# Optimization experiments

Hardware: AMD Instinct MI355X
Metric: run time of the kernel (lower is better)

## Reference

```python
import jax, jax.numpy as jnp
import numpy as np

# config (mirrors init_kwargs)
P_DROP = 0.5          # patch_dropout_proba
MIN_F, MAX_F = 0.1, 0.5  # min/max fraction of patches dropped
B, C, H, W = 64, 64, 128, 128
KH, KW = 8, 8
HP, WP = H // KH, W // KW   # 16, 16 (zero leftout padding since H%KH==0)
PQ = HP * WP                # 256 patches per image


def setup_inputs() -> dict:
    key = jax.random.key(0)
    kb, ke = jax.random.split(key)
    batch = jax.random.normal(kb, (B, C, H, W), dtype=jnp.float32)
    # patch_dropout_embed: torch used 2*(rand(1,C,KH,KW)-0.5) expanded to PQ copies;
    # stored here as an independent (PQ, C, KH, KW) parameter tensor.
    embed = 2.0 * (jax.random.uniform(ke, (PQ, C, KH, KW), dtype=jnp.float32) - 0.5)
    return {"batch": batch, "embed": embed}


def _swap_mask(key):
    """Vectorized per-image patch-drop mask [B, PQ] (replaces python batch loop)."""
    k1, k2, k3 = jax.random.split(key, 3)
    apply = jax.random.uniform(k1, (B,)) < P_DROP                       # per-image coin flip
    frac = jax.random.uniform(k2, (B,)) * (MAX_F - MIN_F) + MIN_F       # dropped fraction
    dropped = jnp.floor(frac * PQ).astype(jnp.int32)                    # int(frac * patch_qty)
    r = jax.random.uniform(k3, (B, PQ))
    ranks = jnp.argsort(jnp.argsort(r, axis=-1), axis=-1)               # random permutation ranks
    return (ranks < dropped[:, None]) & apply[:, None]


def reference(batch, embed):
    mask = _swap_mask(jax.random.key(42))                               # [B, PQ]
    # tile image into patches: [B, C, HP, WP, KH, KW]
    x = batch.reshape(B, C, HP, KH, WP, KW).transpose(0, 1, 2, 4, 3, 5)
    # embed.permute(1,0,2,3).view(C, HP, WP, KH, KW) from the torch code
    e = embed.transpose(1, 0, 2, 3).reshape(C, HP, WP, KH, KW)
    m = mask.reshape(B, 1, HP, WP, 1, 1)
    out = jnp.where(m, e[None], x)
    return out.transpose(0, 1, 2, 4, 3, 5).reshape(B, C, H, W)
```

## Files before the change

### kernel.cpp

```cpp
#include <hip/hip_runtime.h>
#include <stdint.h>


#define BB 64
#define PQ 256

typedef float f32x4 __attribute__((ext_vector_type(4)));

__device__ __forceinline__ uint32_t rotl32(uint32_t v, int r) {
  return (v << r) | (v >> (32 - r));
}

__device__ __forceinline__ void tf2x32(uint32_t k0, uint32_t k1,
                                       uint32_t x0, uint32_t x1,
                                       uint32_t& o0, uint32_t& o1) {
  uint32_t ks2 = k0 ^ k1 ^ 0x1BD11BDAu;
  x0 += k0; x1 += k1;
#define TFR(r) { x0 += x1; x1 = rotl32(x1, (r)); x1 ^= x0; }
  TFR(13) TFR(15) TFR(26) TFR(6)   x0 += k1;  x1 += ks2 + 1u;
  TFR(17) TFR(29) TFR(16) TFR(24)  x0 += ks2; x1 += k0  + 2u;
  TFR(13) TFR(15) TFR(26) TFR(6)   x0 += k0;  x1 += k1  + 3u;
  TFR(17) TFR(29) TFR(16) TFR(24)  x0 += k1;  x1 += ks2 + 4u;
  TFR(13) TFR(15) TFR(26) TFR(6)   x0 += ks2; x1 += k0  + 5u;
#undef TFR
  o0 = x0; o1 = x1;
}

__device__ __forceinline__ uint32_t tf_fold(uint32_t k0, uint32_t k1,
                                            uint32_t c_hi, uint32_t c_lo) {
  uint32_t a, b;
  tf2x32(k0, k1, c_hi, c_lo, a, b);
  return a ^ b;
}

__device__ __forceinline__ float bits_to_unif(uint32_t bits) {
  return __uint_as_float((bits >> 9) | 0x3f800000u) - 1.0f;
}

__global__ __launch_bounds__(256) void mask_kernel(unsigned char* __restrict__ mask) {
  __shared__ uint32_t keybits[PQ];
  __shared__ int s_dropped;
  __shared__ int s_apply;

  const int b = blockIdx.x;
  const int p = threadIdx.x;

  uint32_t k3a, k3b; tf2x32(0u, 42u, 0u, 2u, k3a, k3b);

  const uint32_t rb = tf_fold(k3a, k3b, 0u, (uint32_t)(b * PQ + p)) >> 9;
  keybits[p] = rb;

  if (p == 0) {
    uint32_t k1a, k1b; tf2x32(0u, 42u, 0u, 0u, k1a, k1b);
    uint32_t k2a, k2b; tf2x32(0u, 42u, 0u, 1u, k2a, k2b);
    float u1 = bits_to_unif(tf_fold(k1a, k1b, 0u, (uint32_t)b));
    float u2 = bits_to_unif(tf_fold(k2a, k2b, 0u, (uint32_t)b));
    s_apply = (u1 < 0.5f) ? 1 : 0;
    float frac = u2 * 0.4f;
    frac = frac + 0.1f;
    s_dropped = (int)floorf(frac * 256.0f);
  }
  __syncthreads();

  int rank = 0;
  for (int q = 0; q < PQ; ++q) {
    uint32_t o = keybits[q];
    rank += (o < rb) || (o == rb && q < p);
  }
  mask[b * PQ + p] = (s_apply && rank < s_dropped) ? 1 : 0;
}

__global__ __launch_bounds__(256) void patch_dropout_kernel(
    const f32x4* __restrict__ batch,
    const f32x4* __restrict__ embed,
    const unsigned char* __restrict__ mask,
    f32x4* __restrict__ out, int n4) {
  int i = blockIdx.x * blockDim.x + threadIdx.x;
  if (i >= n4) return;
  const int w4 = i & 31;
  const int h  = (i >> 5) & 127;
  const int c  = (i >> 12) & 63;
  const int b  = i >> 18;
  const int pq = ((h >> 3) << 4) | (w4 >> 1);

  f32x4 v;
  if (mask[(b << 8) | pq]) {
    v = embed[(pq << 10) + (c << 4) + ((h & 7) << 1) + (w4 & 1)];
  } else {
    v = batch[i];
  }
  __builtin_nontemporal_store(v, &out[i]);
}

extern "C" void kernel_launch(void* const* d_in, const int* in_sizes, int n_in,
                              void* d_out, int out_size, void* d_ws, size_t ws_size,
                              hipStream_t stream) {
  const float* batch = (const float*)d_in[0];
  const float* embed = (const float*)d_in[1];
  float* out = (float*)d_out;
  unsigned char* mask = (unsigned char*)d_ws;

  mask_kernel<<<BB, 256, 0, stream>>>(mask);

  const int n4 = out_size / 4;
  const int blocks = (n4 + 255) / 256;
  patch_dropout_kernel<<<blocks, 256, 0, stream>>>(
      (const f32x4*)batch, (const f32x4*)embed, mask, (f32x4*)out, n4);
}
```

Before: 92.02 us.

## Fuse mask generation into patch dropout kernel with per-block partial rank compute

Drops the separate mask kernel and launch. Each block of the copy kernel computes the mask bits for its 16 patches itself, using a split rank count over shared memory with shuffle reduction, and skips the RNG and rank work when the image is not selected. This removes one kernel launch, the mask round trip through global memory and the serialization between the two kernels. In exchange, every block repeats the Threefry hashing and the partial ranking, and adds barriers to the memory-bound copy path.

Measured after the change: 94.23 us. 1.02x slower.

```diff
diff --git a/kernel.cpp b/kernel.cpp
--- a/kernel.cpp
+++ b/kernel.cpp
@@ -2,8 +2,9 @@
 #include <stdint.h>
 
 
-#define BB 64
 #define PQ 256
+#define MAIN_THREADS 256
+#define MAIN_BLOCKS 65536
 
 typedef float f32x4 __attribute__((ext_vector_type(4)));
 
@@ -37,20 +38,21 @@
   return __uint_as_float((bits >> 9) | 0x3f800000u) - 1.0f;
 }
 
-__global__ __launch_bounds__(256) void mask_kernel(unsigned char* __restrict__ mask) {
+__global__ __launch_bounds__(MAIN_THREADS) void patch_dropout_fused(
+    const f32x4* __restrict__ batch,
+    const f32x4* __restrict__ embed,
+    f32x4* __restrict__ out) {
   __shared__ uint32_t keybits[PQ];
-  __shared__ int s_dropped;
-  __shared__ int s_apply;
+  __shared__ int s_m[16];
+  __shared__ int s_apply, s_dropped;
 
-  const int b = blockIdx.x;
-  const int p = threadIdx.x;
+  const int tid  = threadIdx.x;
+  const int base = blockIdx.x * MAIN_THREADS;
+  const int i    = base + tid;
+  const int b    = i >> 18;
+  const int hp0  = ((base >> 5) & 127) >> 3;
 
-  uint32_t k3a, k3b; tf2x32(0u, 42u, 0u, 2u, k3a, k3b);
-
-  const uint32_t rb = tf_fold(k3a, k3b, 0u, (uint32_t)(b * PQ + p)) >> 9;
-  keybits[p] = rb;
-
-  if (p == 0) {
+  if (tid == 0) {
     uint32_t k1a, k1b; tf2x32(0u, 42u, 0u, 0u, k1a, k1b);
     uint32_t k2a, k2b; tf2x32(0u, 42u, 0u, 1u, k2a, k2b);
     float u1 = bits_to_unif(tf_fold(k1a, k1b, 0u, (uint32_t)b));
@@ -62,29 +64,41 @@
   }
   __syncthreads();
 
-  int rank = 0;
-  for (int q = 0; q < PQ; ++q) {
-    uint32_t o = keybits[q];
-    rank += (o < rb) || (o == rb && q < p);
+  if (s_apply) {
+    uint32_t k3a, k3b; tf2x32(0u, 42u, 0u, 2u, k3a, k3b);
+    keybits[tid] = tf_fold(k3a, k3b, 0u, (uint32_t)(b * PQ + tid)) >> 9;
+    __syncthreads();
+
+    const int j = tid >> 4;
+    const int k = tid & 15;
+    const int pqj = (hp0 << 4) | j;
+    const uint32_t rp = keybits[pqj];
+    int part = 0;
+#pragma unroll
+    for (int qq = 0; qq < 16; ++qq) {
+      const int q = (k << 4) | qq;
+      const uint32_t o = keybits[q];
+      part += (o < rp) || (o == rp && q < pqj);
+    }
+    part += __shfl_xor(part, 1);
+    part += __shfl_xor(part, 2);
+    part += __shfl_xor(part, 4);
+    part += __shfl_xor(part, 8);
+    if (k == 0) s_m[j] = (part < s_dropped) ? 1 : 0;
+    __syncthreads();
+  } else {
+    if (tid < 16) s_m[tid] = 0;
+    __syncthreads();
   }
-  mask[b * PQ + p] = (s_apply && rank < s_dropped) ? 1 : 0;
-}
 
-__global__ __launch_bounds__(256) void patch_dropout_kernel(
-    const f32x4* __restrict__ batch,
-    const f32x4* __restrict__ embed,
-    const unsigned char* __restrict__ mask,
-    f32x4* __restrict__ out, int n4) {
-  int i = blockIdx.x * blockDim.x + threadIdx.x;
-  if (i >= n4) return;
   const int w4 = i & 31;
   const int h  = (i >> 5) & 127;
   const int c  = (i >> 12) & 63;
-  const int b  = i >> 18;
-  const int pq = ((h >> 3) << 4) | (w4 >> 1);
+  const int wp = w4 >> 1;
 
   f32x4 v;
-  if (mask[(b << 8) | pq]) {
+  if (s_m[wp]) {
+    const int pq = (hp0 << 4) | wp;
     v = embed[(pq << 10) + (c << 4) + ((h & 7) << 1) + (w4 & 1)];
   } else {
     v = batch[i];
@@ -98,12 +112,8 @@
   const float* batch = (const float*)d_in[0];
   const float* embed = (const float*)d_in[1];
   float* out = (float*)d_out;
-  unsigned char* mask = (unsigned char*)d_ws;
+  (void)d_ws; (void)ws_size; (void)in_sizes; (void)n_in; (void)out_size;
 
-  mask_kernel<<<BB, 256, 0, stream>>>(mask);
-
-  const int n4 = out_size / 4;
-  const int blocks = (n4 + 255) / 256;
-  patch_dropout_kernel<<<blocks, 256, 0, stream>>>(
-      (const f32x4*)batch, (const f32x4*)embed, mask, (f32x4*)out, n4);
+  patch_dropout_fused<<<MAIN_BLOCKS, MAIN_THREADS, 0, stream>>>(
+      (const f32x4*)batch, (const f32x4*)embed, (f32x4*)out);
 }
```
